# Optimization experiments

Hardware: AMD Instinct MI355X
Metric: run time of the kernel (lower is better)

## Reference

```python
import jax, jax.numpy as jnp
import numpy as np

BITS = 8
EPS = 1e-5


def round_clip(x, lo, hi):
    # round-then-clip with straight-through estimator (matches Audyn's round_clip)
    return x + jax.lax.stop_gradient(jnp.clip(jnp.round(x), lo, hi) - x)


def setup_inputs() -> dict:
    key = jax.random.key(0)
    kx, kw = jax.random.split(key)
    B, S, D_IN, D_OUT = 4, 2048, 4096, 16384
    x = jax.random.normal(kx, (B, S, D_IN), dtype=jnp.float32)
    # kaiming-uniform-ish scale: bound = 1/sqrt(in_features)
    bound = 1.0 / np.sqrt(D_IN)
    weight = jax.random.uniform(kw, (D_OUT, D_IN), dtype=jnp.float32,
                                minval=-bound, maxval=bound)
    return {"x": x, "weight": weight}


def reference(x, weight):
    q = float(2 ** (BITS - 1))  # 128
    # activation quantization: per-tensor abs-max
    gamma = jnp.maximum(jnp.max(jnp.abs(x)), EPS)
    xq = round_clip(x * (q / gamma), -q, q - 1.0)
    # weight quantization: per-tensor mean-abs (NB: source divides abs_weight, not weight)
    abs_w = jnp.abs(weight)
    beta = jnp.maximum(jnp.mean(abs_w), EPS)
    wq = round_clip(abs_w / beta, -1.0, 1.0)
    # GEMM (no bias: source always registers bias as None) + rescale
    y = jnp.einsum("bsd,od->bso", xq, wq)
    return y * (beta * gamma / q)
```

## Files before the change

kernel.cpp:

```cpp
#include <hip/hip_runtime.h>

typedef float f32x4  __attribute__((ext_vector_type(4)));
typedef int   i32x4  __attribute__((ext_vector_type(4)));
typedef int   i32x16 __attribute__((ext_vector_type(16)));
typedef char  s8x16  __attribute__((ext_vector_type(16)));

#define GAS __attribute__((address_space(1)))
#define LAS __attribute__((address_space(3)))
#define SBAR __builtin_amdgcn_sched_barrier(0)

constexpr int M = 8192;
constexpr int N = 16384;
constexpr int K = 4096;
constexpr long long NX = (long long)M * K;
constexpr long long NW = (long long)N * K;
constexpr int NPART = 2048;

constexpr int BKB    = 64;
constexpr int NTT    = K / BKB;
constexpr int ABYTES = 256 * BKB;
constexpr int BBYTES = 128 * BKB;
constexpr int BUFB   = ABYTES + BBYTES;


__global__ void reduce_absmax_kernel(const float* __restrict__ x,
                                     unsigned* __restrict__ gmax, int n4) {
  float m = 0.f;
  int stride = gridDim.x * blockDim.x;
  for (int i = blockIdx.x * blockDim.x + threadIdx.x; i < n4; i += stride) {
    f32x4 v = *(const f32x4*)(x + (size_t)i * 4);
    m = fmaxf(m, fmaxf(fmaxf(fabsf(v[0]), fabsf(v[1])),
                       fmaxf(fabsf(v[2]), fabsf(v[3]))));
  }
#pragma unroll
  for (int off = 32; off > 0; off >>= 1) m = fmaxf(m, __shfl_down(m, off));
  __shared__ float sm[4];
  int lane = threadIdx.x & 63, wid = threadIdx.x >> 6;
  if (lane == 0) sm[wid] = m;
  __syncthreads();
  if (threadIdx.x == 0) {
    m = fmaxf(fmaxf(sm[0], sm[1]), fmaxf(sm[2], sm[3]));
    atomicMax(gmax, __float_as_uint(m));
  }
}

__global__ void reduce_abssum_kernel(const float* __restrict__ w,
                                     float* __restrict__ partials, int n4) {
  float s = 0.f;
  int stride = gridDim.x * blockDim.x;
  for (int i = blockIdx.x * blockDim.x + threadIdx.x; i < n4; i += stride) {
    f32x4 v = *(const f32x4*)(w + (size_t)i * 4);
    s += fabsf(v[0]) + fabsf(v[1]) + fabsf(v[2]) + fabsf(v[3]);
  }
#pragma unroll
  for (int off = 32; off > 0; off >>= 1) s += __shfl_down(s, off);
  __shared__ float sm[4];
  int lane = threadIdx.x & 63, wid = threadIdx.x >> 6;
  if (lane == 0) sm[wid] = s;
  __syncthreads();
  if (threadIdx.x == 0) partials[blockIdx.x] = (sm[0] + sm[1]) + (sm[2] + sm[3]);
}

__global__ void finalize_kernel(const unsigned* __restrict__ gbits,
                                const float* __restrict__ partials,
                                float* __restrict__ params) {
  __shared__ double sd[256];
  double s = 0.0;
  for (int i = threadIdx.x; i < NPART; i += 256) s += (double)partials[i];
  sd[threadIdx.x] = s;
  __syncthreads();
  for (int h = 128; h > 0; h >>= 1) {
    if (threadIdx.x < h) sd[threadIdx.x] += sd[threadIdx.x + h];
    __syncthreads();
  }
  if (threadIdx.x == 0) {
    float beta  = fmaxf((float)(sd[0] / (double)NW), 1e-5f);
    float gamma = fmaxf(__uint_as_float(gbits[0]), 1e-5f);
    params[0] = 128.0f / gamma;
    params[1] = beta;
    params[2] = beta * gamma / 128.0f;
  }
}


__global__ void quant_x_kernel(const float* __restrict__ x,
                               char* __restrict__ xq,
                               const float* __restrict__ params, int n16) {
  float s = params[0];
  int stride = gridDim.x * blockDim.x;
  for (int i = blockIdx.x * blockDim.x + threadIdx.x; i < n16; i += stride) {
    const f32x4* p = (const f32x4*)(x + (size_t)i * 16);
    s8x16 o;
#pragma unroll
    for (int v = 0; v < 4; ++v) {
      f32x4 t = p[v];
#pragma unroll
      for (int k = 0; k < 4; ++k) {
        float r = fminf(fmaxf(rintf(t[k] * s), -128.f), 127.f);
        o[v * 4 + k] = (char)(int)r;
      }
    }
    *(s8x16*)(xq + (size_t)i * 16) = o;
  }
}

__global__ void quant_w_kernel(const float* __restrict__ w,
                               char* __restrict__ wq,
                               const float* __restrict__ params, int n16) {
  float beta = params[1];
  int stride = gridDim.x * blockDim.x;
  for (int i = blockIdx.x * blockDim.x + threadIdx.x; i < n16; i += stride) {
    const f32x4* p = (const f32x4*)(w + (size_t)i * 16);
    s8x16 o;
#pragma unroll
    for (int v = 0; v < 4; ++v) {
      f32x4 t = p[v];
#pragma unroll
      for (int k = 0; k < 4; ++k) {
        o[v * 4 + k] = (rintf(fabsf(t[k]) / beta) >= 1.0f) ? (char)1 : (char)0;
      }
    }
    *(s8x16*)(wq + (size_t)i * 16) = o;
  }
}


__global__ __launch_bounds__(512, 4) void gemm_kernel(
    const char* __restrict__ A,
    const char* __restrict__ B,
    float* __restrict__ C,
    const float* __restrict__ params) {
  __shared__ __align__(16) char lds[3 * BUFB];

  const int tid  = threadIdx.x;
  const int lane = tid & 63, wid = tid >> 6;
  const int wm = wid >> 1, wn = wid & 1;
  const int l31 = lane & 31, h = lane >> 5;

  const int wg = (blockIdx.x & 7) * 512 + (blockIdx.x >> 3);
  const int m0 = (wg >> 7) * 256, n0 = (wg & 127) * 128;

  const int csw = (((lane & 3) ^ ((lane >> 3) & 3))) * 16;
  const char* gA = A + (size_t)(m0 + wid * 32 + (lane >> 2)) * K + csw;
  const char* gB = B + (size_t)(n0 + wid * 16 + (lane >> 2)) * K + csw;
  const int dA = wid * 2048 + lane * 16;
  const int dB = ABYTES + wid * 1024 + lane * 16;

  auto stage = [&](int t, int bo) {
    char* L = lds + bo;
    const char* a = gA + t * BKB;
    __builtin_amdgcn_global_load_lds((const GAS void*)a,              (LAS void*)(L + dA),        16, 0, 0);
    __builtin_amdgcn_global_load_lds((const GAS void*)(a + 16 * K),   (LAS void*)(L + dA + 1024), 16, 0, 0);
    __builtin_amdgcn_global_load_lds((const GAS void*)(gB + t * BKB), (LAS void*)(L + dB),        16, 0, 0);
  };

  const int rsw = (l31 >> 1) & 3;
  int aoff[2][2], boff[2][2];
#pragma unroll
  for (int fm = 0; fm < 2; ++fm)
#pragma unroll
    for (int ks = 0; ks < 2; ++ks)
      aoff[fm][ks] = (wm * 64 + fm * 32 + l31) * BKB + (((ks * 2 + h) ^ rsw) * 16);
#pragma unroll
  for (int fn = 0; fn < 2; ++fn)
#pragma unroll
    for (int ks = 0; ks < 2; ++ks)
      boff[fn][ks] = ABYTES + (wn * 64 + fn * 32 + l31) * BKB + (((ks * 2 + h) ^ rsw) * 16);

  i32x16 acc[2][2] = {};

  auto compute = [&](int bo) {
    const char* buf = lds + bo;
    i32x4 af[2][2], bf[2][2];
#pragma unroll
    for (int fm = 0; fm < 2; ++fm)
#pragma unroll
      for (int ks = 0; ks < 2; ++ks)
        af[fm][ks] = *(const i32x4*)(buf + aoff[fm][ks]);
#pragma unroll
    for (int fn = 0; fn < 2; ++fn)
#pragma unroll
      for (int ks = 0; ks < 2; ++ks)
        bf[fn][ks] = *(const i32x4*)(buf + boff[fn][ks]);
    __builtin_amdgcn_s_setprio(1);
#pragma unroll
    for (int fm = 0; fm < 2; ++fm)
#pragma unroll
      for (int fn = 0; fn < 2; ++fn)
#pragma unroll
        for (int ks = 0; ks < 2; ++ks)
          acc[fm][fn] = __builtin_amdgcn_mfma_i32_32x32x32_i8(af[fm][ks], bf[fn][ks], acc[fm][fn], 0, 0, 0);
    __builtin_amdgcn_s_setprio(0);
  };

  stage(0, 0);
  stage(1, BUFB);

  int cb = 0, sb = 2 * BUFB;
  for (int t = 0; t < NTT - 1; ++t) {
    asm volatile("s_waitcnt vmcnt(3)" ::: "memory");
    SBAR;
    __builtin_amdgcn_s_barrier();
    SBAR;
    if (t + 2 < NTT) stage(t + 2, sb);
    compute(cb);
    cb = (cb == 2 * BUFB) ? 0 : cb + BUFB;
    sb = (sb == 2 * BUFB) ? 0 : sb + BUFB;
  }
  asm volatile("s_waitcnt vmcnt(0)" ::: "memory");
  SBAR;
  __builtin_amdgcn_s_barrier();
  SBAR;
  compute(cb);

  const float sc = params[2];
#pragma unroll
  for (int fm = 0; fm < 2; ++fm)
#pragma unroll
    for (int fn = 0; fn < 2; ++fn) {
      const int crow = m0 + wm * 64 + fm * 32 + h * 4;
      const int ccol = n0 + wn * 64 + fn * 32 + l31;
#pragma unroll
      for (int r = 0; r < 16; ++r) {
        const int row = crow + (r & 3) + 8 * (r >> 2);
        C[(size_t)row * N + ccol] = (float)acc[fm][fn][r] * sc;
      }
    }
}


extern "C" void kernel_launch(void* const* d_in, const int* in_sizes, int n_in,
                              void* d_out, int out_size, void* d_ws, size_t ws_size,
                              hipStream_t stream) {
  const float* x = (const float*)d_in[0];
  const float* w = (const float*)d_in[1];
  float* out = (float*)d_out;
  char* ws = (char*)d_ws;

  unsigned* gamma_bits = (unsigned*)ws;
  float*    params     = (float*)(ws + 16);
  float*    partials   = (float*)(ws + 256);
  char*     xq = ws + 16384;
  char*     wq = ws + 16384 + (size_t)NX;

  hipMemsetAsync(ws, 0, 256, stream);

  reduce_absmax_kernel<<<NPART, 256, 0, stream>>>(x, gamma_bits, (int)(NX / 4));
  reduce_abssum_kernel<<<NPART, 256, 0, stream>>>(w, partials, (int)(NW / 4));
  finalize_kernel<<<1, 256, 0, stream>>>(gamma_bits, partials, params);
  quant_x_kernel<<<2048, 256, 0, stream>>>(x, xq, params, (int)(NX / 16));
  quant_w_kernel<<<2048, 256, 0, stream>>>(w, wq, params, (int)(NW / 16));

  gemm_kernel<<<4096, 512, 0, stream>>>(xq, wq, out, params);
}
```

Baseline: 765.1 us.

## Retile int8 GEMM to 128x128 blocks with K=128 double buffering

Changes the int8 MFMA GEMM from 256x128 tiles with 512 threads, a K-step of 64 and triple-buffered LDS to 128x128 tiles with 256 threads, a K-step of 128 and two 32KB LDS buffers. The LDS swizzle widens to 8 chunks, the block-to-tile mapping is reworked for locality, and fragment reads now finish before the next stage is issued. The aim is fewer loop iterations and barriers, and more blocks in flight. The trade-off is that smaller tiles lower operand reuse, and waiting for all loads before each barrier leaves less load/compute overlap.

```diff
diff --git a/kernel.cpp b/kernel.cpp
--- a/kernel.cpp
+++ b/kernel.cpp
@@ -15,12 +15,7 @@
 constexpr long long NX = (long long)M * K;
 constexpr long long NW = (long long)N * K;
 constexpr int NPART = 2048;
-
-constexpr int BKB    = 64;
-constexpr int NTT    = K / BKB;
-constexpr int ABYTES = 256 * BKB;
-constexpr int BBYTES = 128 * BKB;
-constexpr int BUFB   = ABYTES + BBYTES;
+constexpr int NKT = 32;
 
 
 __global__ void reduce_absmax_kernel(const float* __restrict__ x,
@@ -125,93 +120,78 @@
 }
 
 
-__global__ __launch_bounds__(512, 4) void gemm_kernel(
+__global__ __launch_bounds__(256, 2) void gemm_kernel(
     const char* __restrict__ A,
     const char* __restrict__ B,
     float* __restrict__ C,
     const float* __restrict__ params) {
-  __shared__ __align__(16) char lds[3 * BUFB];
+  __shared__ __align__(16) char lds[65536];
 
   const int tid  = threadIdx.x;
   const int lane = tid & 63, wid = tid >> 6;
-  const int wm = wid >> 1, wn = wid & 1;
+  const int wm = wid & 1, wn = wid >> 1;
   const int l31 = lane & 31, h = lane >> 5;
 
-  const int wg = (blockIdx.x & 7) * 512 + (blockIdx.x >> 3);
-  const int m0 = (wg >> 7) * 256, n0 = (wg & 127) * 128;
-
-  const int csw = (((lane & 3) ^ ((lane >> 3) & 3))) * 16;
-  const char* gA = A + (size_t)(m0 + wid * 32 + (lane >> 2)) * K + csw;
-  const char* gB = B + (size_t)(n0 + wid * 16 + (lane >> 2)) * K + csw;
-  const int dA = wid * 2048 + lane * 16;
-  const int dB = ABYTES + wid * 1024 + lane * 16;
-
-  auto stage = [&](int t, int bo) {
-    char* L = lds + bo;
-    const char* a = gA + t * BKB;
-    __builtin_amdgcn_global_load_lds((const GAS void*)a,              (LAS void*)(L + dA),        16, 0, 0);
-    __builtin_amdgcn_global_load_lds((const GAS void*)(a + 16 * K),   (LAS void*)(L + dA + 1024), 16, 0, 0);
-    __builtin_amdgcn_global_load_lds((const GAS void*)(gB + t * BKB), (LAS void*)(L + dB),        16, 0, 0);
+  const int wg = (blockIdx.x & 7) * 1024 + (blockIdx.x >> 3);
+  const int m0 = ((wg >> 10) * 8 + (wg & 7)) * 128;
+  const int n0 = ((wg & 1023) >> 3) * 128;
+
+  const int csw = ((tid & 7) ^ ((tid >> 3) & 7)) * 16;
+  const char* gA = A + (size_t)(m0 + (tid >> 3)) * K + csw;
+  const char* gB = B + (size_t)(n0 + (tid >> 3)) * K + csw;
+  const int dst = tid * 16;
+
+  auto stage = [&](int t) {
+    char* L = lds + (t & 1) * 32768;
+    const size_t ko = (size_t)t * 128;
+#pragma unroll
+    for (int j = 0; j < 4; ++j) {
+      __builtin_amdgcn_global_load_lds((const GAS void*)(gA + ko + (size_t)j * 32 * K),
+                                       (LAS void*)(L + j * 4096 + dst), 16, 0, 0);
+      __builtin_amdgcn_global_load_lds((const GAS void*)(gB + ko + (size_t)j * 32 * K),
+                                       (LAS void*)(L + 16384 + j * 4096 + dst), 16, 0, 0);
+    }
   };
 
-  const int rsw = (l31 >> 1) & 3;
-  int aoff[2][2], boff[2][2];
-#pragma unroll
-  for (int fm = 0; fm < 2; ++fm)
-#pragma unroll
-    for (int ks = 0; ks < 2; ++ks)
-      aoff[fm][ks] = (wm * 64 + fm * 32 + l31) * BKB + (((ks * 2 + h) ^ rsw) * 16);
-#pragma unroll
-  for (int fn = 0; fn < 2; ++fn)
-#pragma unroll
-    for (int ks = 0; ks < 2; ++ks)
-      boff[fn][ks] = ABYTES + (wn * 64 + fn * 32 + l31) * BKB + (((ks * 2 + h) ^ rsw) * 16);
+  int aoff[2][4], boff[2][4];
+#pragma unroll
+  for (int f = 0; f < 2; ++f)
+#pragma unroll
+    for (int ks = 0; ks < 4; ++ks) {
+      const int sw = (((ks * 2 + h) ^ (l31 & 7)) * 16);
+      aoff[f][ks] = (wm * 64 + f * 32 + l31) * 128 + sw;
+      boff[f][ks] = 16384 + (wn * 64 + f * 32 + l31) * 128 + sw;
+    }
 
   i32x16 acc[2][2] = {};
 
-  auto compute = [&](int bo) {
-    const char* buf = lds + bo;
-    i32x4 af[2][2], bf[2][2];
-#pragma unroll
-    for (int fm = 0; fm < 2; ++fm)
-#pragma unroll
-      for (int ks = 0; ks < 2; ++ks)
-        af[fm][ks] = *(const i32x4*)(buf + aoff[fm][ks]);
-#pragma unroll
-    for (int fn = 0; fn < 2; ++fn)
-#pragma unroll
-      for (int ks = 0; ks < 2; ++ks)
-        bf[fn][ks] = *(const i32x4*)(buf + boff[fn][ks]);
-    __builtin_amdgcn_s_setprio(1);
-#pragma unroll
-    for (int fm = 0; fm < 2; ++fm)
-#pragma unroll
-      for (int fn = 0; fn < 2; ++fn)
-#pragma unroll
-        for (int ks = 0; ks < 2; ++ks)
-          acc[fm][fn] = __builtin_amdgcn_mfma_i32_32x32x32_i8(af[fm][ks], bf[fn][ks], acc[fm][fn], 0, 0, 0);
-    __builtin_amdgcn_s_setprio(0);
-  };
-
-  stage(0, 0);
-  stage(1, BUFB);
-
-  int cb = 0, sb = 2 * BUFB;
-  for (int t = 0; t < NTT - 1; ++t) {
-    asm volatile("s_waitcnt vmcnt(3)" ::: "memory");
+  stage(0);
+
+  for (int t = 0; t < NKT; ++t) {
+    const char* buf = lds + (t & 1) * 32768;
+    asm volatile("s_waitcnt vmcnt(0)" ::: "memory");
     SBAR;
     __builtin_amdgcn_s_barrier();
     SBAR;
-    if (t + 2 < NTT) stage(t + 2, sb);
-    compute(cb);
-    cb = (cb == 2 * BUFB) ? 0 : cb + BUFB;
-    sb = (sb == 2 * BUFB) ? 0 : sb + BUFB;
-  }
-  asm volatile("s_waitcnt vmcnt(0)" ::: "memory");
-  SBAR;
-  __builtin_amdgcn_s_barrier();
-  SBAR;
-  compute(cb);
+    i32x4 af[2][4], bf[2][4];
+#pragma unroll
+    for (int f = 0; f < 2; ++f)
+#pragma unroll
+      for (int ks = 0; ks < 4; ++ks) {
+        af[f][ks] = *(const i32x4*)(buf + aoff[f][ks]);
+        bf[f][ks] = *(const i32x4*)(buf + boff[f][ks]);
+      }
+    if (t + 1 < NKT) stage(t + 1);
+    __builtin_amdgcn_s_setprio(1);
+#pragma unroll
+    for (int ks = 0; ks < 4; ++ks)
+#pragma unroll
+      for (int fm = 0; fm < 2; ++fm)
+#pragma unroll
+        for (int fn = 0; fn < 2; ++fn)
+          acc[fm][fn] = __builtin_amdgcn_mfma_i32_32x32x32_i8(af[fm][ks], bf[fn][ks], acc[fm][fn], 0, 0, 0);
+    __builtin_amdgcn_s_setprio(0);
+  }
 
   const float sc = params[2];
 #pragma unroll
@@ -251,5 +231,5 @@
   quant_x_kernel<<<2048, 256, 0, stream>>>(x, xq, params, (int)(NX / 16));
   quant_w_kernel<<<2048, 256, 0, stream>>>(w, wq, params, (int)(NW / 16));
 
-  gemm_kernel<<<4096, 512, 0, stream>>>(xq, wq, out, params);
-}
+  gemm_kernel<<<8192, 256, 0, stream>>>(xq, wq, out, params);
+}
```

New measurement: 859.2 us. 12.3% more time.
